# Kernel optimization log

Hardware: AMD Instinct MI355X
Metric: run time of the kernel (lower is better)

Reference implementation:

```python
import jax, jax.numpy as jnp
import numpy as np

SEQ, BATCH, IN_CH = 4096, 8, 256
HID = 256
LOOKBACK, LOOKAHEAD = 1, 0
K = LOOKBACK + 1 + LOOKAHEAD  # conv kernel size = 2


def setup_inputs() -> dict:
    key = jax.random.key(0)
    k1, k2, k3, k4, k5, k6 = jax.random.split(key, 6)
    X = jax.random.normal(k1, (SEQ, BATCH, IN_CH), dtype=jnp.float32)
    hidden = jax.random.normal(k2, (BATCH, HID), dtype=jnp.float32)
    scale = 1.0 / np.sqrt(IN_CH * K)
    Wz = jax.random.normal(k3, (HID, IN_CH, K), dtype=jnp.float32) * scale
    bz = jax.random.normal(k4, (HID,), dtype=jnp.float32) * scale
    Wf = jax.random.normal(k5, (HID, IN_CH, K), dtype=jnp.float32) * scale
    bf = jax.random.normal(k6, (HID,), dtype=jnp.float32) * scale
    return {"X": X, "hidden": hidden, "Wz": Wz, "bz": bz, "Wf": Wf, "bf": bf}


def _conv1d(Xp, W, b):
    # Xp: (B, C_in, S_pad); W: (C_out, C_in, K) -> (B, C_out, S)
    y = jax.lax.conv_general_dilated(
        Xp, W, window_strides=(1,), padding='VALID',
        dimension_numbers=('NCW', 'OIW', 'NCW'))
    return y + b[None, :, None]


def reference(X, hidden, Wz, bz, Wf, bf):
    # pad seq dim: lookback zeros in front, lookahead behind
    X_pad = jnp.pad(X, ((LOOKBACK, LOOKAHEAD), (0, 0), (0, 0)))
    Xp = jnp.transpose(X_pad, (1, 2, 0))  # (B, C_in, S_pad)

    Z = jnp.transpose(_conv1d(Xp, Wz, bz), (2, 0, 1))  # (S, B, H)
    F = jnp.transpose(_conv1d(Xp, Wf, bf), (2, 0, 1))  # (S, B, H)

    Z = Z * jax.nn.sigmoid(1.702 * Z)  # QuickGELU
    F = jax.nn.sigmoid(F)

    def step(h, fz):
        f, z = fz
        h = f * z + (1.0 - f) * h
        return h, h

    h_last, H = jax.lax.scan(step, hidden, (F, Z))
    return H, h_last[None]  # (S,B,H), (1,B,H)
```

## Files before the change

kernel.cpp:

```cpp
#include <hip/hip_runtime.h>


#define SEQn 4096
#define NCH 2048
#define CHUNK 32
#define NCHUNK 128

typedef __attribute__((ext_vector_type(8))) short bf16x8;
typedef __attribute__((ext_vector_type(4))) float floatx4;

__device__ __forceinline__ unsigned short f2bf(float x) {
  unsigned int u = __float_as_uint(x);
  u += 0x7fffu + ((u >> 16) & 1u);
  return (unsigned short)(u >> 16);
}
__device__ __forceinline__ float bf2f(ushort u) {
  return __uint_as_float((unsigned int)u << 16);
}
__device__ __forceinline__ float sigf(float x) {
  return 1.0f / (1.0f + __expf(-x));
}

__global__ void pack_x_kernel(const float* __restrict__ X, ushort* __restrict__ Xbf) {
  int idx = blockIdx.x * blockDim.x + threadIdx.x;
  const int total4 = ((SEQn + 1) * NCH) / 4;
  if (idx >= total4) return;
  const int pad4 = NCH / 4;
  float4 v;
  if (idx < pad4) { v.x = 0.f; v.y = 0.f; v.z = 0.f; v.w = 0.f; }
  else v = ((const float4*)X)[idx - pad4];
  ushort4 o;
  o.x = f2bf(v.x); o.y = f2bf(v.y); o.z = f2bf(v.z); o.w = f2bf(v.w);
  ((ushort4*)Xbf)[idx] = o;
}

__global__ void pack_w_kernel(const float* __restrict__ Wz, const float* __restrict__ Wf,
                              ushort* __restrict__ Bm) {
  int idx = blockIdx.x * blockDim.x + threadIdx.x;
  if (idx >= 512 * 512) return;
  int n = idx >> 9, kin = idx & 511;
  const float* W = (n < 256) ? Wz : Wf;
  int h = n & 255, c = kin & 255, tap = kin >> 8;
  Bm[idx] = f2bf(W[h * 512 + c * 2 + tap]);
}

__global__ __launch_bounds__(256) void gemm_kernel(
    const ushort* __restrict__ Xbf, const ushort* __restrict__ Bm,
    const float* __restrict__ bz, const float* __restrict__ bfb,
    ushort* __restrict__ zout, ushort* __restrict__ fout) {
  __shared__ __align__(16) ushort smem[8192];
  ushort* sA = smem;
  ushort* sB = smem + 4096;
  const int tid  = threadIdx.x;
  const int wave = tid >> 6;
  const int lane = tid & 63;
  const int quad = lane >> 4;
  const int lrow = lane & 15;
  const int wm = wave >> 1;
  const int wn = wave & 1;
  const int bm = blockIdx.x;
  const int bn = blockIdx.y;

  floatx4 acc[4][4];
#pragma unroll
  for (int i = 0; i < 4; ++i)
#pragma unroll
    for (int j = 0; j < 4; ++j)
      acc[i][j] = (floatx4){0.f, 0.f, 0.f, 0.f};

  const int mr0 = tid >> 2;
  const int ks  = (tid & 3) * 8;
  const size_t aRow0 = (size_t)(bm * 128 + mr0) * 256;
  const size_t aRow1 = (size_t)(bm * 128 + 64 + mr0) * 256;
  const size_t bRow0 = (size_t)(bn * 128 + mr0) * 512;
  const size_t bRow1 = (size_t)(bn * 128 + 64 + mr0) * 512;
  char* ldsA0 = (char*)sA + wave * 1024;
  char* ldsA1 = (char*)sA + 4096 + wave * 1024;
  char* ldsB0 = (char*)sB + wave * 1024;
  char* ldsB1 = (char*)sB + 4096 + wave * 1024;

  for (int k0 = 0; k0 < 512; k0 += 32) {
    const int kk = k0 + ks;
    const int cA = (kk < 256) ? kk : kk + 1792;
    __syncthreads();
    __builtin_amdgcn_global_load_lds(
        (const __attribute__((address_space(1))) void*)(Xbf + aRow0 + cA),
        (__attribute__((address_space(3))) void*)ldsA0, 16, 0, 0);
    __builtin_amdgcn_global_load_lds(
        (const __attribute__((address_space(1))) void*)(Xbf + aRow1 + cA),
        (__attribute__((address_space(3))) void*)ldsA1, 16, 0, 0);
    __builtin_amdgcn_global_load_lds(
        (const __attribute__((address_space(1))) void*)(Bm + bRow0 + kk),
        (__attribute__((address_space(3))) void*)ldsB0, 16, 0, 0);
    __builtin_amdgcn_global_load_lds(
        (const __attribute__((address_space(1))) void*)(Bm + bRow1 + kk),
        (__attribute__((address_space(3))) void*)ldsB1, 16, 0, 0);
    __syncthreads();

    bf16x8 af[4], bfr[4];
#pragma unroll
    for (int fi = 0; fi < 4; ++fi)
      af[fi] = *(const bf16x8*)&sA[(wm * 64 + fi * 16 + lrow) * 32 + quad * 8];
#pragma unroll
    for (int fj = 0; fj < 4; ++fj)
      bfr[fj] = *(const bf16x8*)&sB[(wn * 64 + fj * 16 + lrow) * 32 + quad * 8];
#pragma unroll
    for (int fi = 0; fi < 4; ++fi)
#pragma unroll
      for (int fj = 0; fj < 4; ++fj)
        acc[fi][fj] = __builtin_amdgcn_mfma_f32_16x16x32_bf16(af[fi], bfr[fj], acc[fi][fj], 0, 0, 0);
  }

  const bool isZ = (bn < 2);
  ushort* gout = isZ ? zout : fout;
  const int ncol0 = (bn & 1) * 128;
  const float* bias = isZ ? bz : bfb;
  float bv[4];
#pragma unroll
  for (int fj = 0; fj < 4; ++fj)
    bv[fj] = bias[ncol0 + wn * 64 + fj * 16 + lrow];

  for (int round = 0; round < 2; ++round) {
    __syncthreads();
    if (wm == round) {
#pragma unroll
      for (int fi = 0; fi < 4; ++fi)
#pragma unroll
        for (int fj = 0; fj < 4; ++fj)
#pragma unroll
          for (int r = 0; r < 4; ++r) {
            float v = acc[fi][fj][r] + bv[fj];
            float o = isZ ? (v * sigf(1.702f * v)) : sigf(v);
            smem[(fi * 16 + quad * 4 + r) * 128 + wn * 64 + fj * 16 + lrow] = f2bf(o);
          }
    }
    __syncthreads();
#pragma unroll
    for (int it = 0; it < 4; ++it) {
      int e = tid + it * 256;
      int row = e >> 4, seg = e & 15;
      uint4 v = *(uint4*)&smem[row * 128 + seg * 8];
      *(uint4*)(gout + (size_t)(bm * 128 + round * 64 + row) * 256 + ncol0 + seg * 8) = v;
    }
  }
}

__global__ void scanA_kernel(const ushort* __restrict__ z, const ushort* __restrict__ f,
                             float* __restrict__ Ac, float* __restrict__ Cc) {
  int t = blockIdx.x * blockDim.x + threadIdx.x;
  int ch = t & (NCH - 1);
  int j = t >> 11;
  const ushort* zp = z + (size_t)j * CHUNK * NCH + ch;
  const ushort* fp = f + (size_t)j * CHUNK * NCH + ch;
  float A = 1.0f, C = 0.0f;
#pragma unroll
  for (int i = 0; i < CHUNK; ++i) {
    float fv = bf2f(fp[(size_t)i * NCH]);
    float zv = bf2f(zp[(size_t)i * NCH]);
    float a = 1.0f - fv;
    C = fmaf(a, C, fv * zv);
    A *= a;
  }
  Ac[t] = A;
  Cc[t] = C;
}

__global__ void scanB_kernel(const float* __restrict__ hidden,
                             const float* __restrict__ Ac, const float* __restrict__ Cc,
                             float* __restrict__ Hs) {
  const int lane = threadIdx.x & 63;
  const int ch = blockIdx.x * 4 + (threadIdx.x >> 6);
  const int j0 = 2 * lane, j1 = 2 * lane + 1;
  float a0 = Ac[j0 * NCH + ch], c0 = Cc[j0 * NCH + ch];
  float a1 = Ac[j1 * NCH + ch], c1 = Cc[j1 * NCH + ch];
  float a = a0 * a1;
  float c = fmaf(a1, c0, c1);
#pragma unroll
  for (int d = 1; d < 64; d <<= 1) {
    float pa = __shfl_up(a, d, 64);
    float pc = __shfl_up(c, d, 64);
    if (lane >= d) { c = fmaf(a, pc, c); a *= pa; }
  }
  float xa = __shfl_up(a, 1, 64), xc = __shfl_up(c, 1, 64);
  if (lane == 0) { xa = 1.0f; xc = 0.0f; }
  float h0 = hidden[ch];
  float hs0 = fmaf(xa, h0, xc);
  Hs[j0 * NCH + ch] = hs0;
  Hs[j1 * NCH + ch] = fmaf(a0, hs0, c0);
}

__global__ void scanC_kernel(const ushort* __restrict__ z, const ushort* __restrict__ f,
                             const float* __restrict__ Hs, float* __restrict__ out) {
  int t = blockIdx.x * blockDim.x + threadIdx.x;
  int ch = t & (NCH - 1);
  int j = t >> 11;
  float h = Hs[t];
  const ushort* zp = z + (size_t)j * CHUNK * NCH + ch;
  const ushort* fp = f + (size_t)j * CHUNK * NCH + ch;
  float* op = out + (size_t)j * CHUNK * NCH + ch;
#pragma unroll
  for (int i = 0; i < CHUNK; ++i) {
    float fv = bf2f(fp[(size_t)i * NCH]);
    float zv = bf2f(zp[(size_t)i * NCH]);
    h = fmaf(fv, zv - h, h);
    op[(size_t)i * NCH] = h;
  }
  if (j == NCHUNK - 1) out[(size_t)SEQn * NCH + ch] = h;
}

extern "C" void kernel_launch(void* const* d_in, const int* in_sizes, int n_in,
                              void* d_out, int out_size, void* d_ws, size_t ws_size,
                              hipStream_t stream) {
  const float* X      = (const float*)d_in[0];
  const float* hidden = (const float*)d_in[1];
  const float* Wz     = (const float*)d_in[2];
  const float* bz     = (const float*)d_in[3];
  const float* Wf     = (const float*)d_in[4];
  const float* bfb    = (const float*)d_in[5];
  float* out = (float*)d_out;

  char* ws = (char*)d_ws;
  ushort* zbf = (ushort*)ws;
  ushort* fbf = (ushort*)(ws + 16777216);
  ushort* Xbf = (ushort*)(ws + 33554432);
  ushort* Bm  = (ushort*)(ws + 50335744);
  float* Ac = (float*)(ws + 33554432);
  float* Cc = (float*)(ws + 34603008);
  float* Hs = (float*)(ws + 35651584);

  pack_x_kernel<<<8194, 256, 0, stream>>>(X, Xbf);
  pack_w_kernel<<<1024, 256, 0, stream>>>(Wz, Wf, Bm);
  dim3 ggrid(256, 4);
  gemm_kernel<<<ggrid, 256, 0, stream>>>(Xbf, Bm, bz, bfb, zbf, fbf);
  scanA_kernel<<<1024, 256, 0, stream>>>(zbf, fbf, Ac, Cc);
  scanB_kernel<<<512, 256, 0, stream>>>(hidden, Ac, Cc, Hs);
  scanC_kernel<<<1024, 256, 0, stream>>>(zbf, fbf, Hs, out);
}
```

Measured before the change: 160.1 us.

## Fuse pack kernels, widen GEMM K-tile with swizzled LDS, vectorize scans

Merges the X and W packing kernels into one launch to drop a launch. The GEMM now loads 64-wide K tiles into 32KB of LDS with an XOR swizzle to avoid bank conflicts, halving the number of sync rounds, and pads the epilogue transpose buffer to a 136-element row stride. Both scan passes process two channels per thread with ushort2/float2 accesses to widen memory transactions. sigmoid uses a hardware reciprocal, which may slightly change rounding; the larger LDS footprint may reduce occupancy.

```diff
diff --git a/kernel.cpp b/kernel.cpp
--- a/kernel.cpp
+++ b/kernel.cpp
@@ -18,39 +18,41 @@
   return __uint_as_float((unsigned int)u << 16);
 }
 __device__ __forceinline__ float sigf(float x) {
-  return 1.0f / (1.0f + __expf(-x));
-}
-
-__global__ void pack_x_kernel(const float* __restrict__ X, ushort* __restrict__ Xbf) {
-  int idx = blockIdx.x * blockDim.x + threadIdx.x;
-  const int total4 = ((SEQn + 1) * NCH) / 4;
-  if (idx >= total4) return;
-  const int pad4 = NCH / 4;
-  float4 v;
-  if (idx < pad4) { v.x = 0.f; v.y = 0.f; v.z = 0.f; v.w = 0.f; }
-  else v = ((const float4*)X)[idx - pad4];
-  ushort4 o;
-  o.x = f2bf(v.x); o.y = f2bf(v.y); o.z = f2bf(v.z); o.w = f2bf(v.w);
-  ((ushort4*)Xbf)[idx] = o;
-}
-
-__global__ void pack_w_kernel(const float* __restrict__ Wz, const float* __restrict__ Wf,
-                              ushort* __restrict__ Bm) {
-  int idx = blockIdx.x * blockDim.x + threadIdx.x;
-  if (idx >= 512 * 512) return;
-  int n = idx >> 9, kin = idx & 511;
-  const float* W = (n < 256) ? Wz : Wf;
-  int h = n & 255, c = kin & 255, tap = kin >> 8;
-  Bm[idx] = f2bf(W[h * 512 + c * 2 + tap]);
+  return __builtin_amdgcn_rcpf(1.0f + __expf(-x));
+}
+
+__global__ void pack_kernel(const float* __restrict__ X,
+                            const float* __restrict__ Wz, const float* __restrict__ Wf,
+                            ushort* __restrict__ Xbf, ushort* __restrict__ Bm) {
+  if (blockIdx.x < 1024) {
+    int idx = blockIdx.x * 256 + threadIdx.x;
+    int n = idx >> 9, kin = idx & 511;
+    const float* W = (n < 256) ? Wz : Wf;
+    int h = n & 255, c = kin & 255, tap = kin >> 8;
+    Bm[idx] = f2bf(W[h * 512 + c * 2 + tap]);
+  } else {
+    int idx = (blockIdx.x - 1024) * 256 + threadIdx.x;
+    const int total4 = ((SEQn + 1) * NCH) / 4;
+    if (idx >= total4) return;
+    const int pad4 = NCH / 4;
+    float4 v;
+    if (idx < pad4) { v.x = 0.f; v.y = 0.f; v.z = 0.f; v.w = 0.f; }
+    else v = ((const float4*)X)[idx - pad4];
+    ushort4 o;
+    o.x = f2bf(v.x); o.y = f2bf(v.y); o.z = f2bf(v.z); o.w = f2bf(v.w);
+    ((ushort4*)Xbf)[idx] = o;
+  }
 }
 
 __global__ __launch_bounds__(256) void gemm_kernel(
     const ushort* __restrict__ Xbf, const ushort* __restrict__ Bm,
     const float* __restrict__ bz, const float* __restrict__ bfb,
     ushort* __restrict__ zout, ushort* __restrict__ fout) {
-  __shared__ __align__(16) ushort smem[8192];
-  ushort* sA = smem;
-  ushort* sB = smem + 4096;
+  __shared__ __align__(16) char smem_raw[32768];
+  ushort* sA = (ushort*)smem_raw;
+  ushort* sB = (ushort*)(smem_raw + 16384);
+  ushort* sT = (ushort*)smem_raw;
+
   const int tid  = threadIdx.x;
   const int wave = tid >> 6;
   const int lane = tid & 63;
@@ -68,47 +70,58 @@
     for (int j = 0; j < 4; ++j)
       acc[i][j] = (floatx4){0.f, 0.f, 0.f, 0.f};
 
-  const int mr0 = tid >> 2;
-  const int ks  = (tid & 3) * 8;
-  const size_t aRow0 = (size_t)(bm * 128 + mr0) * 256;
-  const size_t aRow1 = (size_t)(bm * 128 + 64 + mr0) * 256;
-  const size_t bRow0 = (size_t)(bn * 128 + mr0) * 512;
-  const size_t bRow1 = (size_t)(bn * 128 + 64 + mr0) * 512;
-  char* ldsA0 = (char*)sA + wave * 1024;
-  char* ldsA1 = (char*)sA + 4096 + wave * 1024;
-  char* ldsB0 = (char*)sB + wave * 1024;
-  char* ldsB1 = (char*)sB + 4096 + wave * 1024;
-
-  for (int k0 = 0; k0 < 512; k0 += 32) {
-    const int kk = k0 + ks;
-    const int cA = (kk < 256) ? kk : kk + 1792;
-    __syncthreads();
-    __builtin_amdgcn_global_load_lds(
-        (const __attribute__((address_space(1))) void*)(Xbf + aRow0 + cA),
-        (__attribute__((address_space(3))) void*)ldsA0, 16, 0, 0);
-    __builtin_amdgcn_global_load_lds(
-        (const __attribute__((address_space(1))) void*)(Xbf + aRow1 + cA),
-        (__attribute__((address_space(3))) void*)ldsA1, 16, 0, 0);
-    __builtin_amdgcn_global_load_lds(
-        (const __attribute__((address_space(1))) void*)(Bm + bRow0 + kk),
-        (__attribute__((address_space(3))) void*)ldsB0, 16, 0, 0);
-    __builtin_amdgcn_global_load_lds(
-        (const __attribute__((address_space(1))) void*)(Bm + bRow1 + kk),
-        (__attribute__((address_space(3))) void*)ldsB1, 16, 0, 0);
-    __syncthreads();
-
-    bf16x8 af[4], bfr[4];
-#pragma unroll
-    for (int fi = 0; fi < 4; ++fi)
-      af[fi] = *(const bf16x8*)&sA[(wm * 64 + fi * 16 + lrow) * 32 + quad * 8];
-#pragma unroll
-    for (int fj = 0; fj < 4; ++fj)
-      bfr[fj] = *(const bf16x8*)&sB[(wn * 64 + fj * 16 + lrow) * 32 + quad * 8];
-#pragma unroll
-    for (int fi = 0; fi < 4; ++fi)
-#pragma unroll
-      for (int fj = 0; fj < 4; ++fj)
-        acc[fi][fj] = __builtin_amdgcn_mfma_f32_16x16x32_bf16(af[fi], bfr[fj], acc[fi][fj], 0, 0, 0);
+  int rowS[4], gko[4];
+#pragma unroll
+  for (int it = 0; it < 4; ++it) {
+    int g = wave * 256 + it * 64 + lane;
+    int row = g >> 3, ks8 = g & 7;
+    rowS[it] = row;
+    gko[it] = (ks8 ^ (row & 7)) * 8;
+  }
+  char* ldsA = (char*)sA + wave * 4096 + (lane << 4);
+  char* ldsB = (char*)sB + wave * 4096 + (lane << 4);
+
+  for (int k0 = 0; k0 < 512; k0 += 64) {
+    __syncthreads();
+#pragma unroll
+    for (int it = 0; it < 4; ++it) {
+      const int kk = k0 + gko[it];
+      const int cA = (kk < 256) ? kk : kk + 1792;
+      __builtin_amdgcn_global_load_lds(
+          (const __attribute__((address_space(1))) void*)(Xbf + (size_t)(bm * 128 + rowS[it]) * 256 + cA),
+          (__attribute__((address_space(3))) void*)(ldsA + it * 1024), 16, 0, 0);
+      __builtin_amdgcn_global_load_lds(
+          (const __attribute__((address_space(1))) void*)(Bm + (size_t)(bn * 128 + rowS[it]) * 512 + kk),
+          (__attribute__((address_space(3))) void*)(ldsB + it * 1024), 16, 0, 0);
+    }
+    __syncthreads();
+
+    bf16x8 af[4][2], bfr[4][2];
+#pragma unroll
+    for (int fi = 0; fi < 4; ++fi) {
+      const int r = wm * 64 + fi * 16 + lrow;
+#pragma unroll
+      for (int ks = 0; ks < 2; ++ks) {
+        const int s = (ks * 4 + quad) ^ (r & 7);
+        af[fi][ks] = *(const bf16x8*)&sA[r * 64 + s * 8];
+      }
+    }
+#pragma unroll
+    for (int fj = 0; fj < 4; ++fj) {
+      const int r = wn * 64 + fj * 16 + lrow;
+#pragma unroll
+      for (int ks = 0; ks < 2; ++ks) {
+        const int s = (ks * 4 + quad) ^ (r & 7);
+        bfr[fj][ks] = *(const bf16x8*)&sB[r * 64 + s * 8];
+      }
+    }
+#pragma unroll
+    for (int ks = 0; ks < 2; ++ks)
+#pragma unroll
+      for (int fi = 0; fi < 4; ++fi)
+#pragma unroll
+        for (int fj = 0; fj < 4; ++fj)
+          acc[fi][fj] = __builtin_amdgcn_mfma_f32_16x16x32_bf16(af[fi][ks], bfr[fj][ks], acc[fi][fj], 0, 0, 0);
   }
 
   const bool isZ = (bn < 2);
@@ -131,7 +144,7 @@
           for (int r = 0; r < 4; ++r) {
             float v = acc[fi][fj][r] + bv[fj];
             float o = isZ ? (v * sigf(1.702f * v)) : sigf(v);
-            smem[(fi * 16 + quad * 4 + r) * 128 + wn * 64 + fj * 16 + lrow] = f2bf(o);
+            sT[(fi * 16 + quad * 4 + r) * 136 + wn * 64 + fj * 16 + lrow] = f2bf(o);
           }
     }
     __syncthreads();
@@ -139,7 +152,7 @@
     for (int it = 0; it < 4; ++it) {
       int e = tid + it * 256;
       int row = e >> 4, seg = e & 15;
-      uint4 v = *(uint4*)&smem[row * 128 + seg * 8];
+      uint4 v = *(uint4*)&sT[row * 136 + seg * 8];
       *(uint4*)(gout + (size_t)(bm * 128 + round * 64 + row) * 256 + ncol0 + seg * 8) = v;
     }
   }
@@ -148,21 +161,24 @@
 __global__ void scanA_kernel(const ushort* __restrict__ z, const ushort* __restrict__ f,
                              float* __restrict__ Ac, float* __restrict__ Cc) {
   int t = blockIdx.x * blockDim.x + threadIdx.x;
-  int ch = t & (NCH - 1);
-  int j = t >> 11;
-  const ushort* zp = z + (size_t)j * CHUNK * NCH + ch;
-  const ushort* fp = f + (size_t)j * CHUNK * NCH + ch;
-  float A = 1.0f, C = 0.0f;
+  int ch2 = t & 1023;
+  int j = t >> 10;
+  const size_t base = (size_t)j * CHUNK * NCH + 2 * ch2;
+  const ushort* zp = z + base;
+  const ushort* fp = f + base;
+  float A0 = 1.0f, C0 = 0.0f, A1 = 1.0f, C1 = 0.0f;
 #pragma unroll
   for (int i = 0; i < CHUNK; ++i) {
-    float fv = bf2f(fp[(size_t)i * NCH]);
-    float zv = bf2f(zp[(size_t)i * NCH]);
-    float a = 1.0f - fv;
-    C = fmaf(a, C, fv * zv);
-    A *= a;
-  }
-  Ac[t] = A;
-  Cc[t] = C;
+    ushort2 fv = *(const ushort2*)(fp + (size_t)i * NCH);
+    ushort2 zv = *(const ushort2*)(zp + (size_t)i * NCH);
+    float f0 = bf2f(fv.x), f1 = bf2f(fv.y);
+    float a0 = 1.0f - f0, a1 = 1.0f - f1;
+    C0 = fmaf(a0, C0, f0 * bf2f(zv.x)); A0 *= a0;
+    C1 = fmaf(a1, C1, f1 * bf2f(zv.y)); A1 *= a1;
+  }
+  float2 Av = {A0, A1}, Cv = {C0, C1};
+  *(float2*)(Ac + (size_t)j * NCH + 2 * ch2) = Av;
+  *(float2*)(Cc + (size_t)j * NCH + 2 * ch2) = Cv;
 }
 
 __global__ void scanB_kernel(const float* __restrict__ hidden,
@@ -192,20 +208,28 @@
 __global__ void scanC_kernel(const ushort* __restrict__ z, const ushort* __restrict__ f,
                              const float* __restrict__ Hs, float* __restrict__ out) {
   int t = blockIdx.x * blockDim.x + threadIdx.x;
-  int ch = t & (NCH - 1);
-  int j = t >> 11;
-  float h = Hs[t];
-  const ushort* zp = z + (size_t)j * CHUNK * NCH + ch;
-  const ushort* fp = f + (size_t)j * CHUNK * NCH + ch;
-  float* op = out + (size_t)j * CHUNK * NCH + ch;
+  int ch2 = t & 1023;
+  int j = t >> 10;
+  float2 hv = *(const float2*)(Hs + (size_t)j * NCH + 2 * ch2);
+  float h0 = hv.x, h1 = hv.y;
+  const size_t base = (size_t)j * CHUNK * NCH + 2 * ch2;
+  const ushort* zp = z + base;
+  const ushort* fp = f + base;
+  float* op = out + base;
 #pragma unroll
   for (int i = 0; i < CHUNK; ++i) {
-    float fv = bf2f(fp[(size_t)i * NCH]);
-    float zv = bf2f(zp[(size_t)i * NCH]);
-    h = fmaf(fv, zv - h, h);
-    op[(size_t)i * NCH] = h;
-  }
-  if (j == NCHUNK - 1) out[(size_t)SEQn * NCH + ch] = h;
+    ushort2 fv = *(const ushort2*)(fp + (size_t)i * NCH);
+    ushort2 zv = *(const ushort2*)(zp + (size_t)i * NCH);
+    float f0 = bf2f(fv.x), f1 = bf2f(fv.y);
+    h0 = fmaf(f0, bf2f(zv.x) - h0, h0);
+    h1 = fmaf(f1, bf2f(zv.y) - h1, h1);
+    float2 o = {h0, h1};
+    *(float2*)(op + (size_t)i * NCH) = o;
+  }
+  if (j == NCHUNK - 1) {
+    float2 o = {h0, h1};
+    *(float2*)(out + (size_t)SEQn * NCH + 2 * ch2) = o;
+  }
 }
 
 extern "C" void kernel_launch(void* const* d_in, const int* in_sizes, int n_in,
@@ -228,11 +252,10 @@
   float* Cc = (float*)(ws + 34603008);
   float* Hs = (float*)(ws + 35651584);
 
-  pack_x_kernel<<<8194, 256, 0, stream>>>(X, Xbf);
-  pack_w_kernel<<<1024, 256, 0, stream>>>(Wz, Wf, Bm);
+  pack_kernel<<<9218, 256, 0, stream>>>(X, Wz, Wf, Xbf, Bm);
   dim3 ggrid(256, 4);
   gemm_kernel<<<ggrid, 256, 0, stream>>>(Xbf, Bm, bz, bfb, zbf, fbf);
-  scanA_kernel<<<1024, 256, 0, stream>>>(zbf, fbf, Ac, Cc);
+  scanA_kernel<<<512, 256, 0, stream>>>(zbf, fbf, Ac, Cc);
   scanB_kernel<<<512, 256, 0, stream>>>(hidden, Ac, Cc, Hs);
-  scanC_kernel<<<1024, 256, 0, stream>>>(zbf, fbf, Hs, out);
-}
+  scanC_kernel<<<512, 256, 0, stream>>>(zbf, fbf, Hs, out);
+}
```

Result: faster. 145.1 us (-9.3%).
